# Kernel tuning notes

Measured on AMD Instinct MI355X. Metric: run time of the kernel, lower is better.

Reference implementation:

```python
import jax, jax.numpy as jnp
import numpy as np
import math

N_NODES = 10000
N_EDGES = 30000
N_FEAT = 128
N_GRAPHS = 50
HEADS = 8
OUT_DIM = 10


def _lin_params(key, fin, fout):
    kw, kb = jax.random.split(key)
    s = 1.0 / math.sqrt(fin)
    w = jax.random.uniform(kw, (fin, fout), jnp.float32, -s, s)
    b = jax.random.uniform(kb, (fout,), jnp.float32, -s, s)
    return w, b


def setup_inputs() -> dict:
    key = jax.random.key(0)
    ks = jax.random.split(key, 20)
    inp = {}
    inp["x"] = jax.random.normal(ks[0], (N_NODES, N_FEAT), jnp.float32)
    inp["edge_index"] = jax.random.randint(ks[1], (2, N_EDGES), 0, N_NODES)
    inp["batch"] = jnp.sort(jax.random.randint(ks[2], (N_NODES,), 0, N_GRAPHS))
    # (fin, out_channels) per layer; internal width = out_channels * HEADS
    dims = [(128, 512), (512, 256), (256, 64)]
    ki = 3
    for i, (fin, cout) in enumerate(dims, 1):
        hc = cout * HEADS
        inp[f"q{i}_w"], inp[f"q{i}_b"] = _lin_params(ks[ki], fin, hc); ki += 1
        inp[f"k{i}_w"], inp[f"k{i}_b"] = _lin_params(ks[ki], fin, hc); ki += 1
        inp[f"v{i}_w"], inp[f"v{i}_b"] = _lin_params(ks[ki], fin, hc); ki += 1
        inp[f"s{i}_w"], inp[f"s{i}_b"] = _lin_params(ks[ki], fin, cout); ki += 1
    inp["gate_w"], inp["gate_b"] = _lin_params(ks[ki], 64, 1); ki += 1
    inp["fc_w"], inp["fc_b"] = _lin_params(ks[ki], 64, OUT_DIM)
    return inp


def _tconv(x, src, dst, qw, qb, kw_, kb_, vw, vb, sw, sb):
    # PyG TransformerConv, heads=HEADS, concat=False (mean over heads), root_weight=True
    N = x.shape[0]
    hc = qw.shape[1]
    C = hc // HEADS
    q = (x @ qw + qb).reshape(N, HEADS, C)
    k = (x @ kw_ + kb_).reshape(N, HEADS, C)
    v = (x @ vw + vb).reshape(N, HEADS, C)
    # per-edge attention logits [E, H]
    alpha = (q[dst] * k[src]).sum(-1) * (1.0 / math.sqrt(C))
    # segment softmax over incoming edges of each destination node
    m = jax.ops.segment_max(alpha, dst, num_segments=N)
    ex = jnp.exp(alpha - m[dst])
    den = jax.ops.segment_sum(ex, dst, num_segments=N)
    w = ex / jnp.maximum(den[dst], 1e-16)
    agg = jax.ops.segment_sum(w[:, :, None] * v[src], dst, num_segments=N)  # [N,H,C]
    return agg.mean(axis=1) + x @ sw + sb


def reference(x, edge_index, batch,
              q1_w, q1_b, k1_w, k1_b, v1_w, v1_b, s1_w, s1_b,
              q2_w, q2_b, k2_w, k2_b, v2_w, v2_b, s2_w, s2_b,
              q3_w, q3_b, k3_w, k3_b, v3_w, v3_b, s3_w, s3_b,
              gate_w, gate_b, fc_w, fc_b):
    src, dst = edge_index[0], edge_index[1]
    h = jax.nn.elu(_tconv(x, src, dst, q1_w, q1_b, k1_w, k1_b, v1_w, v1_b, s1_w, s1_b))
    h = jax.nn.elu(_tconv(h, src, dst, q2_w, q2_b, k2_w, k2_b, v2_w, v2_b, s2_w, s2_b))
    h = jax.nn.elu(_tconv(h, src, dst, q3_w, q3_b, k3_w, k3_b, v3_w, v3_b, s3_w, s3_b))
    # GlobalAttention pooling: softmax(gate) within each graph, weighted sum
    gate = h @ gate_w + gate_b  # [N,1]
    gm = jax.ops.segment_max(gate, batch, num_segments=N_GRAPHS)
    ge = jnp.exp(gate - gm[batch])
    gd = jax.ops.segment_sum(ge, batch, num_segments=N_GRAPHS)
    g = ge / jnp.maximum(gd[batch], 1e-16)
    pooled = jax.ops.segment_sum(g * h, batch, num_segments=N_GRAPHS)  # [G,64]
    return pooled @ fc_w + fc_b
```

## Files before the change

kernel.cpp:

```cpp
#include <hip/hip_runtime.h>
#include <stdint.h>
#include <math.h>

#define NN 10000
#define NE 30000
#define NG 50
#define NH 8

typedef _Float16 f16;
typedef _Float16 f16x2 __attribute__((ext_vector_type(2)));
typedef _Float16 f16x4 __attribute__((ext_vector_type(4)));
typedef _Float16 f16x8 __attribute__((ext_vector_type(8)));
typedef float f32x4 __attribute__((ext_vector_type(4)));

__device__ inline void async16(f16* l, const f16* g) {
    __builtin_amdgcn_global_load_lds((const __attribute__((address_space(1))) void*)g,
                                     (__attribute__((address_space(3))) void*)l, 16, 0, 0);
}

__global__ void hist_kernel(const int* __restrict__ dst, int* __restrict__ deg, int E) {
    int e = blockIdx.x * blockDim.x + threadIdx.x;
    if (e < E) atomicAdd(&deg[dst[e]], 1);
}

__global__ __launch_bounds__(1024) void scan_kernel(const int* __restrict__ deg, int* __restrict__ offs, int n) {
    __shared__ int tmp[1024];
    __shared__ int carry;
    if (threadIdx.x == 0) { carry = 0; offs[0] = 0; }
    __syncthreads();
    for (int base = 0; base < n; base += 1024) {
        int i = base + (int)threadIdx.x;
        int v = (i < n) ? deg[i] : 0;
        tmp[threadIdx.x] = v;
        __syncthreads();
        for (int d = 1; d < 1024; d <<= 1) {
            int t = 0;
            if ((int)threadIdx.x >= d) t = tmp[threadIdx.x - d];
            __syncthreads();
            if ((int)threadIdx.x >= d) tmp[threadIdx.x] += t;
            __syncthreads();
        }
        if (i < n) offs[i + 1] = carry + tmp[threadIdx.x];
        __syncthreads();
        if (threadIdx.x == 0) carry += tmp[1023];
        __syncthreads();
    }
}

__global__ void copy_int(const int* __restrict__ a, int* __restrict__ b, int n) {
    int i = blockIdx.x * blockDim.x + threadIdx.x;
    if (i < n) b[i] = a[i];
}

__global__ void scatter_kernel(const int* __restrict__ src, const int* __restrict__ dst,
                               int* __restrict__ cursor, int* __restrict__ srcCSR, int E) {
    int e = blockIdx.x * blockDim.x + threadIdx.x;
    if (e < E) {
        int p = atomicAdd(&cursor[dst[e]], 1);
        srcCSR[p] = src[e];
    }
}

__global__ void sort_csr(const int* __restrict__ offs, int* __restrict__ srcCSR) {
    int n = blockIdx.x * blockDim.x + threadIdx.x;
    if (n >= NN) return;
    int s = offs[n], e = offs[n + 1];
    for (int i = s + 1; i < e; ++i) {
        int v = srcCSR[i];
        int j = i - 1;
        while (j >= s && srcCSR[j] > v) { srcCSR[j + 1] = srcCSR[j]; --j; }
        srcCSR[j + 1] = v;
    }
}

__global__ void goffs_kernel(const int* __restrict__ batch, int* __restrict__ goffs) {
    int g = threadIdx.x;
    if (g > NG) return;
    int lo = 0, hi = NN;
    while (lo < hi) {
        int mid = (lo + hi) >> 1;
        if (batch[mid] < g) lo = mid + 1; else hi = mid;
    }
    goffs[g] = lo;
}

__global__ void cvt_f16_kernel(const float* __restrict__ in, f16* __restrict__ out, int n) {
    int i = blockIdx.x * blockDim.x + threadIdx.x;
    if (i < n) out[i] = (f16)in[i];
}

__global__ __launch_bounds__(256) void prep2t(const float* __restrict__ W0, int n0,
                                              const float* __restrict__ W1, int n1,
                                              f16* __restrict__ Bt, int K, int Ntot) {
    __shared__ float tile[64][65];
    const int k0 = blockIdx.x * 64;
    const int nb = blockIdx.y * 64;
    const int tid = threadIdx.x;
    const int tn = tid & 63;
    const int t4 = tid >> 6;
#pragma unroll
    for (int i = 0; i < 16; ++i) {
        int kl = t4 + i * 4;
        int n = nb + tn;
        int k = k0 + kl;
        float w = 0.0f;
        if (n < n0) w = W0[(size_t)k * n0 + n];
        else if (n < n0 + n1) w = W1[(size_t)k * n1 + (n - n0)];
        tile[kl][tn] = w;
    }
    __syncthreads();
#pragma unroll
    for (int i = 0; i < 16; ++i) {
        int nl = t4 + i * 4;
        Bt[(size_t)(nb + nl) * K + k0 + tn] = (f16)tile[tn][nl];
    }
}

__global__ void biasK(const float* __restrict__ b0, int n0, const float* __restrict__ b1, int n1,
                      float* __restrict__ bias, int Ntot) {
    int n = blockIdx.x * 256 + threadIdx.x;
    if (n < Ntot) bias[n] = (n < n0) ? b0[n] : ((n < n0 + n1) ? b1[n - n0] : 0.0f);
}

__global__ __launch_bounds__(256) void prepU(const float* __restrict__ qw, const float* __restrict__ qb,
                                             const float* __restrict__ kw, const float* __restrict__ kb,
                                             f16* __restrict__ BtY, float* __restrict__ biasY,
                                             int fin, int hc, int C) {
    const int wid = blockIdx.x * 4 + ((int)threadIdx.x >> 6);
    const int lane = threadIdx.x & 63;
    if (wid >= fin * 16) return;
    const int k = wid >> 4;
    const int idx = wid & 15;
    const int h = idx & 7, isV = idx >> 3;
    const float* W = isV ? kw : qw;
    const float* bvec = isV ? qb : kb;
    float s = 0.0f;
    for (int c = lane; c < C; c += 64) s += W[(size_t)k * hc + h * C + c] * bvec[h * C + c];
#pragma unroll
    for (int o = 32; o > 0; o >>= 1) s += __shfl_down(s, o, 64);
    if (lane == 0) BtY[(size_t)(8 * fin + isV * 8 + h) * fin + k] = (f16)s;
    if (wid < 8) {
        float cc = 0.0f;
        for (int c = lane; c < C; c += 64) cc += qb[wid * C + c] * kb[wid * C + c];
#pragma unroll
        for (int o = 32; o > 0; o >>= 1) cc += __shfl_down(cc, o, 64);
        if (lane == 0) biasY[8 * fin + wid] = cc;
    }
}

__global__ __launch_bounds__(256) void prepZB(const float* __restrict__ vw, const float* __restrict__ sw,
                                              const float* __restrict__ vb, f16* __restrict__ Bt2) {
    __shared__ f16 tile[32][65];
    const int k0 = blockIdx.x * 32, c0 = blockIdx.y * 64;
    const int tid = threadIdx.x;
#pragma unroll
    for (int i = 0; i < 8; ++i) {
        int idx = tid + i * 256;
        int kl = idx >> 6, cl = idx & 63;
        int k = k0 + kl, c = c0 + cl;
        float v = 0.0f;
        if (k < 1024)      v = vw[(size_t)(k & 127) * 4096 + (k >> 7) * 512 + c];
        else if (k < 1152) v = sw[(size_t)(k - 1024) * 512 + c];
        else if (k < 1160) v = vb[(k - 1152) * 512 + c];
        tile[kl][cl] = (f16)v;
    }
    __syncthreads();
    const int cl = tid >> 2, kl = (tid & 3) * 8;
    f16x8 v;
#pragma unroll
    for (int t = 0; t < 8; ++t) v[t] = tile[kl + t][cl];
    *(f16x8*)(Bt2 + (size_t)(c0 + cl) * 1184 + k0 + kl) = v;
}

__global__ __launch_bounds__(256) void gemm128(const f16* __restrict__ A, int lda, int zA,
                                               const f16* __restrict__ Bt, int ldb, int zB,
                                               const float* __restrict__ bias,
                                               f16* __restrict__ C, int ldc, int zC,
                                               float* __restrict__ Sf,
                                               int M, int Np, int K, int hcS, int Sw, int act) {
    __shared__ f16 smem[24576];
    const int rm = blockIdx.x * 128;
    if (rm >= M) return;
    A  += (size_t)blockIdx.z * zA;
    Bt += (size_t)blockIdx.z * zB;
    C  += (size_t)blockIdx.z * zC;
    const int tid  = threadIdx.x;
    const int lane = tid & 63;
    const int wave = tid >> 6;
    const int l16  = lane & 15;
    const int quad = lane >> 4;
    const int cn   = blockIdx.y * 128;
    const int wrow = (wave >> 1) * 64;
    const int wcol = (wave & 1) * 64;

    const int rS  = tid >> 2;
    const int kc  = ((tid & 3) ^ ((tid >> 3) & 3)) << 3;
    int rowA0 = rm + rS;       if (rowA0 >= M) rowA0 = M - 1;
    int rowA1 = rm + rS + 64;  if (rowA1 >= M) rowA1 = M - 1;
    const f16* gA0 = A + (size_t)rowA0 * lda + kc;
    const f16* gA1 = A + (size_t)rowA1 * lda + kc;
    const f16* gB0 = Bt + (size_t)(cn + rS) * ldb + kc;
    const f16* gB1 = Bt + (size_t)(cn + rS + 64) * ldb + kc;

    const int swf = (l16 >> 1) & 3;
    const int rdAoff = (wrow + l16) * 32 + ((quad ^ swf) << 3);
    const int rdBoff = 4096 + (wcol + l16) * 32 + ((quad ^ swf) << 3);

    f32x4 acc[4][4] = {};

    auto stage_load = [&](int slot) {
        f16* base = smem + slot * 8192;
        async16(base + tid * 8, gA0);
        async16(base + tid * 8 + 2048, gA1);
        async16(base + 4096 + tid * 8, gB0);
        async16(base + 4096 + tid * 8 + 2048, gB1);
        gA0 += 32; gA1 += 32; gB0 += 32; gB1 += 32;
    };

    const int NI = K >> 5;
    stage_load(0);
    stage_load(1);

    int slot = 0;
    for (int i = 0; i < NI; ++i) {
        if (i + 1 < NI) asm volatile("s_waitcnt vmcnt(4)" ::: "memory");
        else            asm volatile("s_waitcnt vmcnt(0)" ::: "memory");
        asm volatile("s_barrier" ::: "memory");
        if (i + 2 < NI) {
            int s2 = slot + 2; if (s2 >= 3) s2 -= 3;
            stage_load(s2);
        }
        const f16* sb = smem + slot * 8192;
        f16x8 av[4], bv[4];
#pragma unroll
        for (int ii = 0; ii < 4; ++ii) av[ii] = *(const f16x8*)(sb + rdAoff + ii * 512);
#pragma unroll
        for (int j = 0; j < 4; ++j) bv[j] = *(const f16x8*)(sb + rdBoff + j * 512);
#pragma unroll
        for (int ii = 0; ii < 4; ++ii)
#pragma unroll
            for (int j = 0; j < 4; ++j)
                acc[ii][j] = __builtin_amdgcn_mfma_f32_16x16x32_f16(bv[j], av[ii], acc[ii][j], 0, 0, 0);
        ++slot; if (slot == 3) slot = 0;
    }
    __syncthreads();

    f16* sC = smem;
    for (int round = 0; round < 2; ++round) {
        if ((wave >> 1) == round) {
#pragma unroll
            for (int j = 0; j < 4; ++j) {
                const int cb = wcol + j * 16 + quad * 4;
                const float4 bb = *(const float4*)(bias + cn + cb);
#pragma unroll
                for (int i = 0; i < 4; ++i) {
                    const int r = i * 16 + l16;
                    float v0 = acc[i][j][0] + bb.x;
                    float v1 = acc[i][j][1] + bb.y;
                    float v2 = acc[i][j][2] + bb.z;
                    float v3 = acc[i][j][3] + bb.w;
                    if (act) {
                        v0 = v0 > 0.0f ? v0 : (__expf(v0) - 1.0f);
                        v1 = v1 > 0.0f ? v1 : (__expf(v1) - 1.0f);
                        v2 = v2 > 0.0f ? v2 : (__expf(v2) - 1.0f);
                        v3 = v3 > 0.0f ? v3 : (__expf(v3) - 1.0f);
                    }
                    f16x4 o;
                    o[0] = (f16)v0; o[1] = (f16)v1; o[2] = (f16)v2; o[3] = (f16)v3;
                    *(f16x4*)(sC + r * 136 + cb) = o;
                    if (Sf) {
                        const int sc = cn + cb - hcS;
                        if (sc >= 0 && sc < Sw) {
                            const int grow = rm + round * 64 + r;
                            if (grow < M) {
                                float4 sv = { v0, v1, v2, v3 };
                                *(float4*)(Sf + (size_t)grow * Sw + sc) = sv;
                            }
                        }
                    }
                }
            }
        }
        __syncthreads();
#pragma unroll
        for (int it = 0; it < 4; ++it) {
            const int r = it * 16 + (tid >> 4);
            const int ch = tid & 15;
            const int grow = rm + round * 64 + r;
            if (grow < M) {
                f16x8 v = *(const f16x8*)(sC + r * 136 + ch * 8);
                *(f16x8*)(C + (size_t)grow * ldc + cn + ch * 8) = v;
            }
        }
        __syncthreads();
    }
}

__global__ __launch_bounds__(256) void alpha_fused_y(const f16* __restrict__ Y, const f16* __restrict__ X,
                                                     const int* __restrict__ offs,
                                                     const int* __restrict__ srcCSR,
                                                     float* __restrict__ alphaW,
                                                     int strideY, int fin, float scale) {
    const int n = blockIdx.x;
    const int e0 = offs[n];
    int d = offs[n + 1] - e0;
    if (d > 256) d = 256;

    __shared__ __align__(16) f16 sy[1024];
    __shared__ float sew[256 * NH];
    __shared__ float sv[256 * NH];
    __shared__ int sed[256];
    __shared__ float su[NH];
    const int tid = threadIdx.x;

    const f16* Yn = Y + (size_t)n * strideY;
    for (int c = tid; c < fin; c += 256) ((f16x8*)sy)[c] = ((const f16x8*)Yn)[c];
    if (tid < NH) su[tid] = (float)Yn[8 * fin + tid];
    for (int e = tid; e < d; e += 256) {
        int s = srcCSR[e0 + e];
        sed[e] = s;
        f16x8 vv = *(const f16x8*)(Y + (size_t)s * strideY + 8 * fin + 8);
#pragma unroll
        for (int t = 0; t < 8; ++t) sv[e * NH + t] = (float)vv[t];
    }
    __syncthreads();

    const int wv = tid >> 6, lane = tid & 63;
    const int cph = fin >> 3;
    const int csh = __ffs(cph) - 1;
    const int passes = fin >> 6;
    for (int e = wv; e < d; e += 4) {
        const f16x8* kg = (const f16x8*)(X + (size_t)sed[e] * fin);
        for (int p = 0; p < passes; ++p) {
            const int ci = p * 64 + lane;
            const int head = ci >> csh;
            const int kcn = ci & (cph - 1);
            f16x8 yv = ((const f16x8*)sy)[ci];
            f16x8 xv = kg[kcn];
            float acc = 0.0f;
#pragma unroll
            for (int t = 0; t < 8; ++t) acc += (float)yv[t] * (float)xv[t];
            for (int o = cph >> 1; o > 0; o >>= 1) acc += __shfl_down(acc, o, cph);
            if ((lane & (cph - 1)) == 0)
                sew[e * NH + head] = (acc + su[head] + sv[e * NH + head]) * scale;
        }
    }
    __syncthreads();

    if (tid < NH) {
        const int h = tid;
        float m = -3.0e38f;
        for (int e = 0; e < d; ++e) m = fmaxf(m, sew[e * NH + h]);
        float den = 0.0f;
        for (int e = 0; e < d; ++e) {
            float ex = __expf(sew[e * NH + h] - m);
            sew[e * NH + h] = ex;
            den += ex;
        }
        float inv = 1.0f / (fmaxf(den, 1e-16f) * (float)NH);
        for (int e = 0; e < d; ++e) sew[e * NH + h] *= inv;
    }
    __syncthreads();

    for (int i = tid; i < d * NH; i += 256) alphaW[(size_t)e0 * NH + i] = sew[i];
}

__global__ __launch_bounds__(256) void z_agg(const f16* __restrict__ X,
                                             const int* __restrict__ offs,
                                             const int* __restrict__ srcCSR,
                                             const float* __restrict__ alphaW,
                                             f16* __restrict__ Z) {
    const int n = blockIdx.x;
    const int e0 = offs[n];
    int d = offs[n + 1] - e0;
    if (d > 256) d = 256;

    __shared__ float sew[256 * NH];
    __shared__ int sed[256];
    __shared__ __align__(16) f16 sx[32 * 128];
    const int tid = threadIdx.x;

    for (int i = tid; i < d * NH; i += 256) sew[i] = alphaW[(size_t)e0 * NH + i];
    for (int e = tid; e < d; e += 256) sed[e] = srcCSR[e0 + e];
    __syncthreads();

    const int h = tid >> 5;
    const int f0 = (tid * 4) & 127;
    float a0 = 0.0f, a1 = 0.0f, a2 = 0.0f, a3 = 0.0f;
    for (int ch = 0; ch < d; ch += 32) {
        const int cnt = min(32, d - ch);
        for (int idx = tid; idx < cnt * 16; idx += 256) {
            int row = idx >> 4, c8 = idx & 15;
            *(f16x8*)(sx + row * 128 + c8 * 8) = *(const f16x8*)(X + (size_t)sed[ch + row] * 128 + c8 * 8);
        }
        __syncthreads();
        for (int e = 0; e < cnt; ++e) {
            float w = sew[(ch + e) * NH + h];
            f16x4 xv = *(const f16x4*)(sx + e * 128 + f0);
            a0 += w * (float)xv[0];
            a1 += w * (float)xv[1];
            a2 += w * (float)xv[2];
            a3 += w * (float)xv[3];
        }
        __syncthreads();
    }
    f16* Zr = Z + (size_t)n * 1184;
    f16x4 o; o[0] = (f16)a0; o[1] = (f16)a1; o[2] = (f16)a2; o[3] = (f16)a3;
    *(f16x4*)(Zr + tid * 4) = o;
    if (tid < 16) *(f16x8*)(Zr + 1024 + tid * 8) = *(const f16x8*)(X + (size_t)n * 128 + tid * 8);
    if (tid >= 32 && tid < 40) {
        int hh = tid - 32;
        float s = 0.0f;
        for (int e = 0; e < d; ++e) s += sew[e * NH + hh];
        Zr[1152 + hh] = (f16)s;
    }
    if (tid >= 64 && tid < 88) Zr[1160 + (tid - 64)] = (f16)0.0f;
}

__global__ __launch_bounds__(256) void alpha_fused(const f16* __restrict__ QK,
                                                   const int* __restrict__ offs,
                                                   const int* __restrict__ srcCSR,
                                                   float* __restrict__ alphaW,
                                                   int strideQK, int C, int hc, float scale) {
    const int n = blockIdx.x;
    const int e0 = offs[n];
    int d = offs[n + 1] - e0;
    if (d > 256) d = 256;

    __shared__ __align__(16) f16 sq[4096];
    __shared__ float sew[256 * NH];
    __shared__ int sed[256];
    const int tid = threadIdx.x;

    const f16x8* qg = (const f16x8*)(QK + (size_t)n * strideQK);
    const int qchunks = hc >> 3;
    for (int c = tid; c < qchunks; c += 256) ((f16x8*)sq)[c] = qg[c];
    for (int e = tid; e < d; e += 256) sed[e] = srcCSR[e0 + e];
    __syncthreads();

    const int wv = tid >> 6, lane = tid & 63;
    const int cph = C >> 3;
    const int passes = hc >> 9;
    for (int e = wv; e < d; e += 4) {
        const f16x8* kg = (const f16x8*)(QK + (size_t)sed[e] * strideQK + hc);
        for (int p = 0; p < passes; ++p) {
            const int ci = p * 64 + lane;
            f16x8 qv = ((const f16x8*)sq)[ci];
            f16x8 kv = kg[ci];
            float acc = 0.0f;
#pragma unroll
            for (int t = 0; t < 8; ++t) acc += (float)qv[t] * (float)kv[t];
            for (int o = cph >> 1; o > 0; o >>= 1) acc += __shfl_down(acc, o, cph);
            if ((lane & (cph - 1)) == 0) {
                const int head = ci / cph;
                sew[e * NH + head] = acc * scale;
            }
        }
    }
    __syncthreads();

    if (tid < NH) {
        const int h = tid;
        float m = -3.0e38f;
        for (int e = 0; e < d; ++e) m = fmaxf(m, sew[e * NH + h]);
        float den = 0.0f;
        for (int e = 0; e < d; ++e) {
            float ex = __expf(sew[e * NH + h] - m);
            sew[e * NH + h] = ex;
            den += ex;
        }
        float inv = 1.0f / (fmaxf(den, 1e-16f) * (float)NH);
        for (int e = 0; e < d; ++e) sew[e * NH + h] *= inv;
    }
    __syncthreads();

    for (int i = tid; i < d * NH; i += 256) alphaW[(size_t)e0 * NH + i] = sew[i];
}

__global__ __launch_bounds__(256) void node_agg(const f16* __restrict__ VS,
                                                const float* __restrict__ Sf,
                                                const int* __restrict__ offs,
                                                const int* __restrict__ srcCSR,
                                                const float* __restrict__ alphaW,
                                                float* __restrict__ hout, f16* __restrict__ houth,
                                                int C, int hc, int NpVS, int writeHout) {
    const int n = blockIdx.x;
    const int e0 = offs[n];
    int d = offs[n + 1] - e0;
    if (d > 256) d = 256;

    __shared__ float sew[256 * NH];
    __shared__ int sed[256];
    __shared__ float sred[512];
    const int tid = threadIdx.x;

    for (int i = tid; i < d * NH; i += 256) sew[i] = alphaW[(size_t)e0 * NH + i];
    for (int e = tid; e < d; e += 256) sed[e] = srcCSR[e0 + e];
    __syncthreads();

    const int half = C >> 1;
    const int cp = tid & (half - 1);
    const int grp = tid / half;
    const int ngr = 256 / half;
    float a0 = 0.0f, a1 = 0.0f;
    for (int e = grp; e < d; e += ngr) {
        const unsigned int* vp = (const unsigned int*)(VS + (size_t)sed[e] * NpVS);
#pragma unroll
        for (int h = 0; h < NH; ++h) {
            float w = sew[e * NH + h];
            f16x2 vv = __builtin_bit_cast(f16x2, vp[((h * C) >> 1) + cp]);
            a0 += w * (float)vv.x;
            a1 += w * (float)vv.y;
        }
    }
    if (ngr > 1) {
        sred[tid] = a0;
        sred[256 + tid] = a1;
        __syncthreads();
        if (grp == 0) {
            for (int g = 1; g < ngr; ++g) {
                a0 += sred[g * half + cp];
                a1 += sred[256 + g * half + cp];
            }
        }
    }
    if (grp == 0) {
        const int c = cp * 2;
        const float* Sp = Sf + (size_t)n * C;
        float o0 = a0 + Sp[c];
        float o1 = a1 + Sp[c + 1];
        o0 = o0 > 0.0f ? o0 : (__expf(o0) - 1.0f);
        o1 = o1 > 0.0f ? o1 : (__expf(o1) - 1.0f);
        if (writeHout) {
            hout[(size_t)n * C + c] = o0;
            hout[(size_t)n * C + c + 1] = o1;
        }
        houth[(size_t)n * C + c] = (f16)o0;
        houth[(size_t)n * C + c + 1] = (f16)o1;
    }
}

__global__ __launch_bounds__(256) void pool_graph(const float* __restrict__ h,
                                                  const float* __restrict__ gw, const float* __restrict__ gb,
                                                  const float* __restrict__ fcw, const float* __restrict__ fcb,
                                                  const int* __restrict__ goffs,
                                                  float* __restrict__ gbuf, float* __restrict__ out) {
    const int g = blockIdx.x;
    const int s = goffs[g], e = goffs[g + 1];
    const int tid = threadIdx.x;
    const int wv = tid >> 6, lane = tid & 63;

    __shared__ float red[256];
    __shared__ float pl[64];
    __shared__ float sden;

    if (e == s) {
        if (tid < 10) out[g * 10 + tid] = fcb[tid];
        return;
    }

    const float gwl = gw[lane];
    for (int n = s + wv; n < e; n += 4) {
        float acc = h[(size_t)n * 64 + lane] * gwl;
#pragma unroll
        for (int o = 32; o > 0; o >>= 1) acc += __shfl_down(acc, o, 64);
        if (lane == 0) gbuf[n] = acc + gb[0];
    }
    __syncthreads();

    float m = -3.0e38f;
    for (int n = s + tid; n < e; n += 256) m = fmaxf(m, gbuf[n]);
    red[tid] = m;
    __syncthreads();
    for (int o = 128; o > 0; o >>= 1) {
        if (tid < o) red[tid] = fmaxf(red[tid], red[tid + o]);
        __syncthreads();
    }
    m = red[0];
    __syncthreads();

    float sum = 0.0f;
    for (int n = s + tid; n < e; n += 256) {
        float ex = __expf(gbuf[n] - m);
        gbuf[n] = ex;
        sum += ex;
    }
    red[tid] = sum;
    __syncthreads();
    for (int o = 128; o > 0; o >>= 1) {
        if (tid < o) red[tid] += red[tid + o];
        __syncthreads();
    }
    if (tid == 0) sden = 1.0f / fmaxf(red[0], 1e-16f);
    __syncthreads();

    float acc = 0.0f;
    for (int n = s + wv; n < e; n += 4) acc += gbuf[n] * h[(size_t)n * 64 + lane];
    red[tid] = acc;
    __syncthreads();
    if (wv == 0) pl[lane] = (red[lane] + red[64 + lane] + red[128 + lane] + red[192 + lane]) * sden;
    __syncthreads();

    if (tid < 10) {
        float o = fcb[tid];
#pragma unroll
        for (int c = 0; c < 64; ++c) o += pl[c] * fcw[c * 10 + tid];
        out[g * 10 + tid] = o;
    }
}

extern "C" void kernel_launch(void* const* d_in, const int* in_sizes, int n_in,
                              void* d_out, int out_size, void* d_ws, size_t ws_size,
                              hipStream_t stream) {
    const float* x   = (const float*)d_in[0];
    const int* ei    = (const int*)d_in[1];
    const int* src   = ei;
    const int* dst   = ei + NE;
    const int* batch = (const int*)d_in[2];

    struct LayerW { int fin, C, hc; const float *qw,*qb,*kw,*kb,*vw,*vb,*sw,*sb; };
    LayerW LW[3];
    const int fins[3]   = {128, 512, 256};
    const int Cs[3]     = {512, 256, 64};
    const int NpVS[3]   = {0, 2304, 640};
    for (int l = 0; l < 3; ++l) {
        int b = 3 + 8 * l;
        LW[l].fin = fins[l]; LW[l].C = Cs[l]; LW[l].hc = Cs[l] * NH;
        LW[l].qw = (const float*)d_in[b + 0]; LW[l].qb = (const float*)d_in[b + 1];
        LW[l].kw = (const float*)d_in[b + 2]; LW[l].kb = (const float*)d_in[b + 3];
        LW[l].vw = (const float*)d_in[b + 4]; LW[l].vb = (const float*)d_in[b + 5];
        LW[l].sw = (const float*)d_in[b + 6]; LW[l].sb = (const float*)d_in[b + 7];
    }
    const float* gate_w = (const float*)d_in[27];
    const float* gate_b = (const float*)d_in[28];
    const float* fc_w   = (const float*)d_in[29];
    const float* fc_b   = (const float*)d_in[30];

    size_t off = 0;
    char* ws = (char*)d_ws;
    auto alloc = [&](size_t bytes) -> void* {
        void* p = ws + off;
        off = (off + bytes + 255) & ~(size_t)255;
        return p;
    };
    f16* BtQK   = (f16*)alloc((size_t)4096 * 512 * sizeof(f16));
    f16* BtVS   = (f16*)alloc((size_t)2304 * 512 * sizeof(f16));
    float* biasQK = (float*)alloc(8192 * sizeof(float));
    float* biasVS = (float*)alloc(4608 * sizeof(float));
    f16* QKbuf  = (f16*)alloc((size_t)NN * 4608 * sizeof(f16));
    float* Sf   = (float*)alloc((size_t)NN * 512 * sizeof(float));
    f16* xh     = (f16*)alloc((size_t)NN * 128 * sizeof(f16));
    f16* houth  = (f16*)alloc((size_t)NN * 512 * sizeof(f16));
    float* hf   = (float*)alloc((size_t)NN * 64 * sizeof(float));
    float* alphaW = (float*)alloc((size_t)NE * NH * sizeof(float));
    f16* qw16   = (f16*)alloc((size_t)128 * 4096 * sizeof(f16));
    f16* kw16   = (f16*)alloc((size_t)128 * 4096 * sizeof(f16));
    f16* BtY    = (f16*)alloc((size_t)1152 * 128 * sizeof(f16));
    float* biasY = (float*)alloc(1152 * sizeof(float));
    float* zbias = (float*)alloc(512 * sizeof(float));
    int* deg    = (int*)alloc(NN * sizeof(int));
    int* offs   = (int*)alloc((NN + 1) * sizeof(int));
    int* cursor = (int*)alloc(NN * sizeof(int));
    int* srcCSR = (int*)alloc(NE * sizeof(int));
    int* goffs  = (int*)alloc((NG + 1) * sizeof(int));
    float* gbuf = (float*)alloc(NN * sizeof(float));
    if (off > ws_size) return;

    hipMemsetAsync(deg, 0, NN * sizeof(int), stream);
    hipMemsetAsync(zbias, 0, 512 * sizeof(float), stream);
    hipMemsetAsync(biasY, 0, 1152 * sizeof(float), stream);
    hist_kernel<<<(NE + 255) / 256, 256, 0, stream>>>(dst, deg, NE);
    scan_kernel<<<1, 1024, 0, stream>>>(deg, offs, NN);
    copy_int<<<(NN + 255) / 256, 256, 0, stream>>>(offs, cursor, NN);
    scatter_kernel<<<(NE + 255) / 256, 256, 0, stream>>>(src, dst, cursor, srcCSR, NE);
    sort_csr<<<(NN + 255) / 256, 256, 0, stream>>>(offs, srcCSR);
    goffs_kernel<<<1, 64, 0, stream>>>(batch, goffs);

    cvt_f16_kernel<<<(NN * 128 + 255) / 256, 256, 0, stream>>>(x, xh, NN * 128);

    const int grid_m = 80;
    const f16* Acur = xh;
    for (int l = 0; l < 3; ++l) {
        const int K = LW[l].fin, C = LW[l].C, hc = LW[l].hc;
        const float scale = 1.0f / sqrtf((float)C);

        if (l == 0) {
            const int fin = 128, NtotY = 1152;
            cvt_f16_kernel<<<(fin * hc + 255) / 256, 256, 0, stream>>>(LW[0].qw, qw16, fin * hc);
            cvt_f16_kernel<<<(fin * hc + 255) / 256, 256, 0, stream>>>(LW[0].kw, kw16, fin * hc);
            dim3 gm(1, 1, 8);
            gemm128<<<gm, 256, 0, stream>>>(kw16, hc, C, qw16, hc, C, zbias,
                                            BtY, fin, fin * fin, nullptr, fin, fin, C, 0, 0, 0);
            prepU<<<(fin * 16 + 3) / 4, 256, 0, stream>>>(LW[0].qw, LW[0].qb, LW[0].kw, LW[0].kb,
                                                          BtY, biasY, fin, hc, C);
            dim3 gy(grid_m, NtotY / 128);
            gemm128<<<gy, 256, 0, stream>>>(xh, fin, 0, BtY, fin, 0, biasY,
                                            QKbuf, NtotY, 0, nullptr, NN, NtotY, fin, 0, 0, 0);
            alpha_fused_y<<<NN, 256, 0, stream>>>(QKbuf, xh, offs, srcCSR, alphaW,
                                                  NtotY, fin, scale);
            z_agg<<<NN, 256, 0, stream>>>(xh, offs, srcCSR, alphaW, QKbuf);
            prepZB<<<dim3(37, 8), 256, 0, stream>>>(LW[0].vw, LW[0].sw, LW[0].vb, BtVS);
            biasK<<<2, 256, 0, stream>>>(LW[0].sb, 512, LW[0].sb, 0, biasVS, 512);
            dim3 gz(grid_m, 4);
            gemm128<<<gz, 256, 0, stream>>>(QKbuf, 1184, 0, BtVS, 1184, 0, biasVS,
                                            houth, 512, 0, nullptr, NN, 512, 1184, 0, 0, 1);
        } else {
            const int Np0 = 2 * hc, Np1 = NpVS[l];
            prep2t<<<dim3(K / 64, Np0 / 64), 256, 0, stream>>>(LW[l].qw, hc, LW[l].kw, hc,
                                                               BtQK, K, Np0);
            biasK<<<(Np0 + 255) / 256, 256, 0, stream>>>(LW[l].qb, hc, LW[l].kb, hc, biasQK, Np0);
            dim3 gqk(grid_m, Np0 / 128);
            gemm128<<<gqk, 256, 0, stream>>>(Acur, K, 0, BtQK, K, 0, biasQK,
                                             QKbuf, Np0, 0, nullptr, NN, Np0, K, 0, 0, 0);
            alpha_fused<<<NN, 256, 0, stream>>>(QKbuf, offs, srcCSR, alphaW, Np0, C, hc, scale);

            prep2t<<<dim3(K / 64, Np1 / 64), 256, 0, stream>>>(LW[l].vw, hc, LW[l].sw, C,
                                                               BtVS, K, Np1);
            biasK<<<(Np1 + 255) / 256, 256, 0, stream>>>(LW[l].vb, hc, LW[l].sb, C, biasVS, Np1);
            dim3 gvs(grid_m, Np1 / 128);
            gemm128<<<gvs, 256, 0, stream>>>(Acur, K, 0, BtVS, K, 0, biasVS,
                                             QKbuf, Np1, 0, Sf, NN, Np1, K, hc, C, 0);

            node_agg<<<NN, 256, 0, stream>>>(QKbuf, Sf, offs, srcCSR, alphaW, hf, houth,
                                             C, hc, Np1, l == 2 ? 1 : 0);
        }
        Acur = houth;
    }

    pool_graph<<<NG, 256, 0, stream>>>(hf, gate_w, gate_b, fc_w, fc_b, goffs, gbuf, (float*)d_out);
}
```

Before: 565.0 us.

## Fuse QKVS projections into one GEMM and merge small setup kernels

For layers 2 and 3, the Q, K, V and skip weights are packed into one transposed weight matrix, so a single GEMM computes all projections instead of two separate GEMMs. Bias preparation is folded into the weight-transpose kernels. The scan, cursor copy and graph-offset search are merged into one launch, and the three f16 conversions into another, with the memsets combined into a single span. This cuts launch count and lets the activation tile be read once for all projections, at the cost of a larger output buffer and a wider row stride for the downstream alpha and aggregation kernels.

```diff
diff --git a/kernel.cpp b/kernel.cpp
--- a/kernel.cpp
+++ b/kernel.cpp
@@ -23,33 +23,48 @@
     if (e < E) atomicAdd(&deg[dst[e]], 1);
 }
 
-__global__ __launch_bounds__(1024) void scan_kernel(const int* __restrict__ deg, int* __restrict__ offs, int n) {
-    __shared__ int tmp[1024];
-    __shared__ int carry;
-    if (threadIdx.x == 0) { carry = 0; offs[0] = 0; }
-    __syncthreads();
-    for (int base = 0; base < n; base += 1024) {
-        int i = base + (int)threadIdx.x;
-        int v = (i < n) ? deg[i] : 0;
-        tmp[threadIdx.x] = v;
-        __syncthreads();
-        for (int d = 1; d < 1024; d <<= 1) {
-            int t = 0;
-            if ((int)threadIdx.x >= d) t = tmp[threadIdx.x - d];
-            __syncthreads();
-            if ((int)threadIdx.x >= d) tmp[threadIdx.x] += t;
-            __syncthreads();
-        }
-        if (i < n) offs[i + 1] = carry + tmp[threadIdx.x];
-        __syncthreads();
-        if (threadIdx.x == 0) carry += tmp[1023];
-        __syncthreads();
-    }
-}
-
-__global__ void copy_int(const int* __restrict__ a, int* __restrict__ b, int n) {
-    int i = blockIdx.x * blockDim.x + threadIdx.x;
-    if (i < n) b[i] = a[i];
+__global__ __launch_bounds__(1024) void scan_goffs(const int* __restrict__ deg, int* __restrict__ offs,
+                                                   int* __restrict__ cursor,
+                                                   const int* __restrict__ batch, int* __restrict__ goffs) {
+    if (blockIdx.x == 1) {
+        int g = threadIdx.x;
+        if (g > NG) return;
+        int lo = 0, hi = NN;
+        while (lo < hi) {
+            int mid = (lo + hi) >> 1;
+            if (batch[mid] < g) lo = mid + 1; else hi = mid;
+        }
+        goffs[g] = lo;
+        return;
+    }
+    __shared__ int tot[1024];
+    const int t = threadIdx.x;
+    const int base = t * 10;
+    int v[10];
+    int s = 0;
+#pragma unroll
+    for (int i = 0; i < 10; ++i) {
+        int idx = base + i;
+        v[i] = (idx < NN) ? deg[idx] : 0;
+        s += v[i];
+    }
+    tot[t] = s;
+    __syncthreads();
+    for (int d2 = 1; d2 < 1024; d2 <<= 1) {
+        int add = (t >= d2) ? tot[t - d2] : 0;
+        __syncthreads();
+        tot[t] += add;
+        __syncthreads();
+    }
+    int run = tot[t] - s;
+    if (t == 0) offs[0] = 0;
+#pragma unroll
+    for (int i = 0; i < 10; ++i) {
+        int idx = base + i;
+        if (idx < NN) cursor[idx] = run;
+        run += v[i];
+        if (idx < NN) offs[idx + 1] = run;
+    }
 }
 
 __global__ void scatter_kernel(const int* __restrict__ src, const int* __restrict__ dst,
@@ -73,25 +88,23 @@
     }
 }
 
-__global__ void goffs_kernel(const int* __restrict__ batch, int* __restrict__ goffs) {
-    int g = threadIdx.x;
-    if (g > NG) return;
-    int lo = 0, hi = NN;
-    while (lo < hi) {
-        int mid = (lo + hi) >> 1;
-        if (batch[mid] < g) lo = mid + 1; else hi = mid;
-    }
-    goffs[g] = lo;
-}
-
-__global__ void cvt_f16_kernel(const float* __restrict__ in, f16* __restrict__ out, int n) {
+__global__ void cvt3_kernel(const float* __restrict__ a, f16* __restrict__ ao, int na,
+                            const float* __restrict__ b, f16* __restrict__ bo, int nb2,
+                            const float* __restrict__ c, f16* __restrict__ co, int nc) {
     int i = blockIdx.x * blockDim.x + threadIdx.x;
-    if (i < n) out[i] = (f16)in[i];
-}
-
-__global__ __launch_bounds__(256) void prep2t(const float* __restrict__ W0, int n0,
+    if (i < na) ao[i] = (f16)a[i];
+    else if (i < na + nb2) { int j = i - na; bo[j] = (f16)b[j]; }
+    else if (i < na + nb2 + nc) { int j = i - na - nb2; co[j] = (f16)c[j]; }
+}
+
+__global__ __launch_bounds__(256) void prep4t(const float* __restrict__ W0, int n0,
                                               const float* __restrict__ W1, int n1,
-                                              f16* __restrict__ Bt, int K, int Ntot) {
+                                              const float* __restrict__ W2, int n2,
+                                              const float* __restrict__ W3, int n3,
+                                              const float* __restrict__ b0, const float* __restrict__ b1,
+                                              const float* __restrict__ b2, const float* __restrict__ b3,
+                                              f16* __restrict__ Bt, float* __restrict__ bias,
+                                              int K, int Ntot) {
     __shared__ float tile[64][65];
     const int k0 = blockIdx.x * 64;
     const int nb = blockIdx.y * 64;
@@ -101,12 +114,33 @@
 #pragma unroll
     for (int i = 0; i < 16; ++i) {
         int kl = t4 + i * 4;
+        int k = k0 + kl;
         int n = nb + tn;
-        int k = k0 + kl;
         float w = 0.0f;
-        if (n < n0) w = W0[(size_t)k * n0 + n];
-        else if (n < n0 + n1) w = W1[(size_t)k * n1 + (n - n0)];
+        int m = n;
+        if (m < n0) w = W0[(size_t)k * n0 + m];
+        else { m -= n0;
+            if (m < n1) w = W1[(size_t)k * n1 + m];
+            else { m -= n1;
+                if (m < n2) w = W2[(size_t)k * n2 + m];
+                else { m -= n2; if (m < n3) w = W3[(size_t)k * n3 + m]; }
+            }
+        }
         tile[kl][tn] = w;
+    }
+    if (blockIdx.x == 0 && t4 == 0) {
+        int n = nb + tn;
+        float bv = 0.0f;
+        int m = n;
+        if (m < n0) bv = b0[m];
+        else { m -= n0;
+            if (m < n1) bv = b1[m];
+            else { m -= n1;
+                if (m < n2) bv = b2[m];
+                else { m -= n2; if (m < n3) bv = b3[m]; }
+            }
+        }
+        bias[n] = bv;
     }
     __syncthreads();
 #pragma unroll
@@ -114,12 +148,6 @@
         int nl = t4 + i * 4;
         Bt[(size_t)(nb + nl) * K + k0 + tn] = (f16)tile[tn][nl];
     }
-}
-
-__global__ void biasK(const float* __restrict__ b0, int n0, const float* __restrict__ b1, int n1,
-                      float* __restrict__ bias, int Ntot) {
-    int n = blockIdx.x * 256 + threadIdx.x;
-    if (n < Ntot) bias[n] = (n < n0) ? b0[n] : ((n < n0 + n1) ? b1[n - n0] : 0.0f);
 }
 
 __global__ __launch_bounds__(256) void prepU(const float* __restrict__ qw, const float* __restrict__ qb,
@@ -149,7 +177,8 @@
 }
 
 __global__ __launch_bounds__(256) void prepZB(const float* __restrict__ vw, const float* __restrict__ sw,
-                                              const float* __restrict__ vb, f16* __restrict__ Bt2) {
+                                              const float* __restrict__ vb, const float* __restrict__ sb,
+                                              f16* __restrict__ Bt2, float* __restrict__ biasZ) {
     __shared__ f16 tile[32][65];
     const int k0 = blockIdx.x * 32, c0 = blockIdx.y * 64;
     const int tid = threadIdx.x;
@@ -164,6 +193,7 @@
         else if (k < 1160) v = vb[(k - 1152) * 512 + c];
         tile[kl][cl] = (f16)v;
     }
+    if (blockIdx.x == 0 && tid < 64) biasZ[c0 + tid] = sb[c0 + tid];
     __syncthreads();
     const int cl = tid >> 2, kl = (tid & 3) * 8;
     f16x8 v;
@@ -483,7 +513,7 @@
                                                 const int* __restrict__ srcCSR,
                                                 const float* __restrict__ alphaW,
                                                 float* __restrict__ hout, f16* __restrict__ houth,
-                                                int C, int hc, int NpVS, int writeHout) {
+                                                int C, int NpVS, int writeHout) {
     const int n = blockIdx.x;
     const int e0 = offs[n];
     int d = offs[n + 1] - e0;
@@ -620,9 +650,8 @@
 
     struct LayerW { int fin, C, hc; const float *qw,*qb,*kw,*kb,*vw,*vb,*sw,*sb; };
     LayerW LW[3];
-    const int fins[3]   = {128, 512, 256};
-    const int Cs[3]     = {512, 256, 64};
-    const int NpVS[3]   = {0, 2304, 640};
+    const int fins[3] = {128, 512, 256};
+    const int Cs[3]   = {512, 256, 64};
     for (int l = 0; l < 3; ++l) {
         int b = 3 + 8 * l;
         LW[l].fin = fins[l]; LW[l].C = Cs[l]; LW[l].hc = Cs[l] * NH;
@@ -643,12 +672,12 @@
         off = (off + bytes + 255) & ~(size_t)255;
         return p;
     };
-    f16* BtQK   = (f16*)alloc((size_t)4096 * 512 * sizeof(f16));
-    f16* BtVS   = (f16*)alloc((size_t)2304 * 512 * sizeof(f16));
-    float* biasQK = (float*)alloc(8192 * sizeof(float));
-    float* biasVS = (float*)alloc(4608 * sizeof(float));
-    f16* QKbuf  = (f16*)alloc((size_t)NN * 4608 * sizeof(f16));
-    float* Sf   = (float*)alloc((size_t)NN * 512 * sizeof(float));
+    f16* BtQK   = (f16*)alloc((size_t)6400 * 512 * sizeof(f16));
+    f16* BtVS   = (f16*)alloc((size_t)512 * 1184 * sizeof(f16));
+    float* biasQK = (float*)alloc(6400 * sizeof(float));
+    float* biasVS = (float*)alloc(512 * sizeof(float));
+    f16* QKbuf  = (f16*)alloc((size_t)NN * 6400 * sizeof(f16));
+    float* Sf   = (float*)alloc((size_t)NN * 256 * sizeof(float));
     f16* xh     = (f16*)alloc((size_t)NN * 128 * sizeof(f16));
     f16* houth  = (f16*)alloc((size_t)NN * 512 * sizeof(f16));
     float* hf   = (float*)alloc((size_t)NN * 64 * sizeof(float));
@@ -656,9 +685,10 @@
     f16* qw16   = (f16*)alloc((size_t)128 * 4096 * sizeof(f16));
     f16* kw16   = (f16*)alloc((size_t)128 * 4096 * sizeof(f16));
     f16* BtY    = (f16*)alloc((size_t)1152 * 128 * sizeof(f16));
+    int*   deg   = (int*)alloc(NN * sizeof(int));
+    float* zbias = (float*)alloc(512 * sizeof(float));
     float* biasY = (float*)alloc(1152 * sizeof(float));
-    float* zbias = (float*)alloc(512 * sizeof(float));
-    int* deg    = (int*)alloc(NN * sizeof(int));
+    size_t zspan = (size_t)((char*)(biasY + 1152) - (char*)deg);
     int* offs   = (int*)alloc((NN + 1) * sizeof(int));
     int* cursor = (int*)alloc(NN * sizeof(int));
     int* srcCSR = (int*)alloc(NE * sizeof(int));
@@ -666,17 +696,18 @@
     float* gbuf = (float*)alloc(NN * sizeof(float));
     if (off > ws_size) return;
 
-    hipMemsetAsync(deg, 0, NN * sizeof(int), stream);
-    hipMemsetAsync(zbias, 0, 512 * sizeof(float), stream);
-    hipMemsetAsync(biasY, 0, 1152 * sizeof(float), stream);
+    hipMemsetAsync(deg, 0, zspan, stream);
     hist_kernel<<<(NE + 255) / 256, 256, 0, stream>>>(dst, deg, NE);
-    scan_kernel<<<1, 1024, 0, stream>>>(deg, offs, NN);
-    copy_int<<<(NN + 255) / 256, 256, 0, stream>>>(offs, cursor, NN);
+    scan_goffs<<<2, 1024, 0, stream>>>(deg, offs, cursor, batch, goffs);
     scatter_kernel<<<(NE + 255) / 256, 256, 0, stream>>>(src, dst, cursor, srcCSR, NE);
     sort_csr<<<(NN + 255) / 256, 256, 0, stream>>>(offs, srcCSR);
-    goffs_kernel<<<1, 64, 0, stream>>>(batch, goffs);
-
-    cvt_f16_kernel<<<(NN * 128 + 255) / 256, 256, 0, stream>>>(x, xh, NN * 128);
+
+    {
+        int na = NN * 128, nb2 = 128 * 4096, nc = 128 * 4096;
+        cvt3_kernel<<<(na + nb2 + nc + 255) / 256, 256, 0, stream>>>(x, xh, na,
+                                                                     LW[0].qw, qw16, nb2,
+                                                                     LW[0].kw, kw16, nc);
+    }
 
     const int grid_m = 80;
     const f16* Acur = xh;
@@ -686,8 +717,6 @@
 
         if (l == 0) {
             const int fin = 128, NtotY = 1152;
-            cvt_f16_kernel<<<(fin * hc + 255) / 256, 256, 0, stream>>>(LW[0].qw, qw16, fin * hc);
-            cvt_f16_kernel<<<(fin * hc + 255) / 256, 256, 0, stream>>>(LW[0].kw, kw16, fin * hc);
             dim3 gm(1, 1, 8);
             gemm128<<<gm, 256, 0, stream>>>(kw16, hc, C, qw16, hc, C, zbias,
                                             BtY, fin, fin * fin, nullptr, fin, fin, C, 0, 0, 0);
@@ -699,30 +728,23 @@
             alpha_fused_y<<<NN, 256, 0, stream>>>(QKbuf, xh, offs, srcCSR, alphaW,
                                                   NtotY, fin, scale);
             z_agg<<<NN, 256, 0, stream>>>(xh, offs, srcCSR, alphaW, QKbuf);
-            prepZB<<<dim3(37, 8), 256, 0, stream>>>(LW[0].vw, LW[0].sw, LW[0].vb, BtVS);
-            biasK<<<2, 256, 0, stream>>>(LW[0].sb, 512, LW[0].sb, 0, biasVS, 512);
+            prepZB<<<dim3(37, 8), 256, 0, stream>>>(LW[0].vw, LW[0].sw, LW[0].vb, LW[0].sb,
+                                                    BtVS, biasVS);
             dim3 gz(grid_m, 4);
             gemm128<<<gz, 256, 0, stream>>>(QKbuf, 1184, 0, BtVS, 1184, 0, biasVS,
                                             houth, 512, 0, nullptr, NN, 512, 1184, 0, 0, 1);
         } else {
-            const int Np0 = 2 * hc, Np1 = NpVS[l];
-            prep2t<<<dim3(K / 64, Np0 / 64), 256, 0, stream>>>(LW[l].qw, hc, LW[l].kw, hc,
-                                                               BtQK, K, Np0);
-            biasK<<<(Np0 + 255) / 256, 256, 0, stream>>>(LW[l].qb, hc, LW[l].kb, hc, biasQK, Np0);
-            dim3 gqk(grid_m, Np0 / 128);
-            gemm128<<<gqk, 256, 0, stream>>>(Acur, K, 0, BtQK, K, 0, biasQK,
-                                             QKbuf, Np0, 0, nullptr, NN, Np0, K, 0, 0, 0);
-            alpha_fused<<<NN, 256, 0, stream>>>(QKbuf, offs, srcCSR, alphaW, Np0, C, hc, scale);
-
-            prep2t<<<dim3(K / 64, Np1 / 64), 256, 0, stream>>>(LW[l].vw, hc, LW[l].sw, C,
-                                                               BtVS, K, Np1);
-            biasK<<<(Np1 + 255) / 256, 256, 0, stream>>>(LW[l].vb, hc, LW[l].sb, C, biasVS, Np1);
-            dim3 gvs(grid_m, Np1 / 128);
-            gemm128<<<gvs, 256, 0, stream>>>(Acur, K, 0, BtVS, K, 0, biasVS,
-                                             QKbuf, Np1, 0, Sf, NN, Np1, K, hc, C, 0);
-
-            node_agg<<<NN, 256, 0, stream>>>(QKbuf, Sf, offs, srcCSR, alphaW, hf, houth,
-                                             C, hc, Np1, l == 2 ? 1 : 0);
+            const int Np = (2 * hc + hc + C + 127) & ~127;
+            prep4t<<<dim3(K / 64, Np / 64), 256, 0, stream>>>(LW[l].qw, hc, LW[l].kw, hc,
+                                                              LW[l].vw, hc, LW[l].sw, C,
+                                                              LW[l].qb, LW[l].kb, LW[l].vb, LW[l].sb,
+                                                              BtQK, biasQK, K, Np);
+            dim3 gq(grid_m, Np / 128);
+            gemm128<<<gq, 256, 0, stream>>>(Acur, K, 0, BtQK, K, 0, biasQK,
+                                            QKbuf, Np, 0, Sf, NN, Np, K, 3 * hc, C, 0);
+            alpha_fused<<<NN, 256, 0, stream>>>(QKbuf, offs, srcCSR, alphaW, Np, C, hc, scale);
+            node_agg<<<NN, 256, 0, stream>>>(QKbuf + 2 * hc, Sf, offs, srcCSR, alphaW, hf, houth,
+                                             C, Np, l == 2 ? 1 : 0);
         }
         Acur = houth;
     }
```

After: 493.0 us. 1.15x faster.
